# Kernel tuning notes

Measured on AMD Instinct MI355X. Metric: run time of the kernel, lower is better.

Reference implementation:

```python
import jax, jax.numpy as jnp
import numpy as np

B_, T_, IN_, H_, N_ = 16, 4096, 2, 256, 256
TWO_PI = 6.283185307179586


def setup_inputs() -> dict:
    key = jax.random.key(0)
    ks = jax.random.split(key, 12)
    x = jax.random.normal(ks[0], (B_, T_, IN_), dtype=jnp.float32)
    lengths = jax.random.randint(ks[1], (B_,), 1, T_ + 1)  # in [1, T]
    # canonical LRU param init (ring init for eigenvalues)
    u1 = jax.random.uniform(ks[2], (N_,))
    u2 = jax.random.uniform(ks[3], (N_,))
    nu_log = jnp.log(-0.5 * jnp.log(u1 * 0.75 + 0.25))          # |lam| in [0.5, 1)
    theta_log = jnp.log(u2 * TWO_PI + 1e-4)
    B_re = jax.random.normal(ks[4], (N_, IN_)) / np.sqrt(2 * IN_)
    B_im = jax.random.normal(ks[5], (N_, IN_)) / np.sqrt(2 * IN_)
    C_re = jax.random.normal(ks[6], (H_, N_)) / np.sqrt(N_)
    C_im = jax.random.normal(ks[7], (H_, N_)) / np.sqrt(N_)
    D = jax.random.normal(ks[8], (H_, IN_))
    Wh = jax.random.normal(ks[9], (1, H_)) / np.sqrt(H_)
    bh = jnp.zeros((1,), dtype=jnp.float32)
    return {"x": x, "lengths": lengths, "nu_log": nu_log.astype(jnp.float32),
            "theta_log": theta_log.astype(jnp.float32), "B_re": B_re.astype(jnp.float32),
            "B_im": B_im.astype(jnp.float32), "C_re": C_re.astype(jnp.float32),
            "C_im": C_im.astype(jnp.float32), "D": D.astype(jnp.float32),
            "Wh": Wh.astype(jnp.float32), "bh": bh}


def _combine(e1, e2):
    a1, b1 = e1
    a2, b2 = e2
    return a1 * a2, a2 * b1 + b2


def reference(x, lengths, nu_log, theta_log, B_re, B_im, C_re, C_im, D, Wh, bh):
    B, T, _ = x.shape
    lam = jnp.exp(-jnp.exp(nu_log) + 1j * jnp.exp(theta_log))          # [N] complex
    gamma = jnp.sqrt(1.0 - jnp.abs(lam) ** 2)                           # [N] real
    Bmat = (B_re + 1j * B_im) * gamma[:, None]                          # [N, IN]
    Bu = jnp.einsum('bti,ni->btn', x.astype(jnp.complex64), Bmat)       # [B,T,N]
    a = jnp.broadcast_to(lam.astype(jnp.complex64), Bu.shape)
    # parallel associative scan of x_t = lam*x_{t-1} + Bu_t along time
    _, states = jax.lax.associative_scan(_combine, (a, Bu), axis=1)     # [B,T,N]
    C = C_re + 1j * C_im                                                # [H,N]
    y = jnp.einsum('btn,hn->bth', states, C).real + x @ D.T             # [B,T,H]
    mask = (jnp.arange(T) < lengths[:, None])[..., None]                # [B,T,1]
    y = y * mask
    last = jnp.take_along_axis(y, (lengths - 1)[:, None, None], axis=1)[:, 0, :]  # [B,H]
    return last @ Wh.T + bh                                             # [B,1]
```

## Files before the change

kernel.cpp:

```cpp
#include <hip/hip_runtime.h>
#include <hip/hip_bf16.h>

#define B_ 16
#define T_ 4096
#define IN_ 2
#define H_ 256
#define N_ 256

#define TWO_PI_F 6.28318530717958647692f
#define INV_TWO_PI_D 0.15915494309189533576888376337251

__global__ __launch_bounds__(256) void cw_kernel(const float* __restrict__ C_re,
                                                 const float* __restrict__ C_im,
                                                 const float* __restrict__ Wh,
                                                 float2* __restrict__ Cw) {
    int n = blockIdx.x;
    int h = threadIdx.x;
    float w = Wh[h];
    float vr = w * C_re[h * N_ + n];
    float vi = w * C_im[h * N_ + n];
    for (int off = 32; off > 0; off >>= 1) {
        vr += __shfl_down(vr, off);
        vi += __shfl_down(vi, off);
    }
    __shared__ float2 sred[4];
    int wid = threadIdx.x >> 6;
    int lane = threadIdx.x & 63;
    if (lane == 0) sred[wid] = make_float2(vr, vi);
    __syncthreads();
    if (threadIdx.x == 0) {
        float2 t = sred[0];
        t.x += sred[1].x + sred[2].x + sred[3].x;
        t.y += sred[1].y + sred[2].y + sred[3].y;
        Cw[n] = t;
    }
}

__global__ __launch_bounds__(256) void lru_kernel(
        const float* __restrict__ x, const int* __restrict__ lengths,
        const float* __restrict__ nu_log, const float* __restrict__ theta_log,
        const float* __restrict__ B_re, const float* __restrict__ B_im,
        const float2* __restrict__ Cw, float* __restrict__ g) {
    const int n = blockIdx.x;
    const int b = blockIdx.y;
    const int tid = threadIdx.x;
    const int tstar = lengths[b] - 1;

    const float nu = __expf(nu_log[n]);
    const float th = __expf(theta_log[n]);
    const double threv = (double)th * INV_TWO_PI_D;

    const float2* xb = ((const float2*)x) + (size_t)b * T_;

    const int k0 = (tstar - tid) & 255;
    const int s0 = tstar - k0;

    double f0 = (double)k0 * threv;
    float ang0 = (float)(f0 - rint(f0)) * TWO_PI_F;
    float sn, cs;
    __sincosf(ang0, &sn, &cs);
    float e0 = __expf(-(float)k0 * nu);
    float fr = e0 * cs, fi = e0 * sn;
    double f2 = 256.0 * threv;
    float ang2 = (float)(f2 - rint(f2)) * TWO_PI_F;
    __sincosf(ang2, &sn, &cs);
    float e2 = __expf(-256.f * nu);
    float rr = e2 * cs, ri = e2 * sn;

    float a0r = 0.f, a0i = 0.f, a1r = 0.f, a1i = 0.f;
#pragma unroll
    for (int j = 0; j < 16; ++j) {
        int s = s0 - 256 * j;
        int sc = s < 0 ? 0 : s;
        float2 xv = xb[sc];
        if (s < 0) { xv.x = 0.f; xv.y = 0.f; }
        a0r = fmaf(fr, xv.x, a0r);
        a0i = fmaf(fi, xv.x, a0i);
        a1r = fmaf(fr, xv.y, a1r);
        a1i = fmaf(fi, xv.y, a1i);
        float nfr = fr * rr - fi * ri;
        float nfi = fmaf(fr, ri, fi * rr);
        fr = nfr;
        fi = nfi;
    }

    for (int off = 32; off > 0; off >>= 1) {
        a0r += __shfl_down(a0r, off);
        a0i += __shfl_down(a0i, off);
        a1r += __shfl_down(a1r, off);
        a1i += __shfl_down(a1i, off);
    }
    __shared__ float4 sred[4];
    int wid = threadIdx.x >> 6;
    int lane = threadIdx.x & 63;
    if (lane == 0) sred[wid] = make_float4(a0r, a0i, a1r, a1i);
    __syncthreads();
    if (threadIdx.x == 0) {
        float4 t = sred[0];
        t.x += sred[1].x + sred[2].x + sred[3].x;
        t.y += sred[1].y + sred[2].y + sred[3].y;
        t.z += sred[1].z + sred[2].z + sred[3].z;
        t.w += sred[1].w + sred[2].w + sred[3].w;
        float gamma = sqrtf(1.f - __expf(-2.f * nu));
        float br0 = B_re[2 * n] * gamma, bi0 = B_im[2 * n] * gamma;
        float br1 = B_re[2 * n + 1] * gamma, bi1 = B_im[2 * n + 1] * gamma;
        float str = t.x * br0 - t.y * bi0 + t.z * br1 - t.w * bi1;
        float sti = t.x * bi0 + t.y * br0 + t.z * bi1 + t.w * br1;
        float2 cw = Cw[n];
        g[b * N_ + n] = str * cw.x - sti * cw.y;
    }
}

__global__ __launch_bounds__(256) void out_kernel(
        const float* __restrict__ g, const float* __restrict__ x,
        const int* __restrict__ lengths, const float* __restrict__ D,
        const float* __restrict__ Wh, const float* __restrict__ bh,
        float* __restrict__ out) {
    int b = blockIdx.x;
    int tstar = lengths[b] - 1;
    int h = threadIdx.x;
    float2 xv = ((const float2*)x)[(size_t)b * T_ + tstar];
    float v = g[b * N_ + h] + Wh[h] * (D[2 * h] * xv.x + D[2 * h + 1] * xv.y);
    for (int off = 32; off > 0; off >>= 1) v += __shfl_down(v, off);
    __shared__ float sred[4];
    int wid = threadIdx.x >> 6;
    int lane = threadIdx.x & 63;
    if (lane == 0) sred[wid] = v;
    __syncthreads();
    if (threadIdx.x == 0) {
        out[b] = sred[0] + sred[1] + sred[2] + sred[3] + bh[0];
    }
}

extern "C" void kernel_launch(void* const* d_in, const int* in_sizes, int n_in,
                              void* d_out, int out_size, void* d_ws, size_t ws_size,
                              hipStream_t stream) {
    const float* x         = (const float*)d_in[0];
    const int*   lengths   = (const int*)d_in[1];
    const float* nu_log    = (const float*)d_in[2];
    const float* theta_log = (const float*)d_in[3];
    const float* B_re      = (const float*)d_in[4];
    const float* B_im      = (const float*)d_in[5];
    const float* C_re      = (const float*)d_in[6];
    const float* C_im      = (const float*)d_in[7];
    const float* D         = (const float*)d_in[8];
    const float* Wh        = (const float*)d_in[9];
    const float* bh        = (const float*)d_in[10];
    float* out = (float*)d_out;

    float2* Cw = (float2*)d_ws;
    float*  g  = (float*)d_ws + 2 * N_;

    cw_kernel<<<N_, 256, 0, stream>>>(C_re, C_im, Wh, Cw);
    lru_kernel<<<dim3(N_, B_), 256, 0, stream>>>(x, lengths, nu_log, theta_log,
                                                 B_re, B_im, Cw, g);
    out_kernel<<<B_, 256, 0, stream>>>(g, x, lengths, D, Wh, bh, out);
}
```

Baseline: 87.50 us.

## Fuse Cw reduction into LRU kernel and process two states per block

```diff
diff --git a/kernel.cpp b/kernel.cpp
--- a/kernel.cpp
+++ b/kernel.cpp
@@ -10,104 +10,117 @@
 #define TWO_PI_F 6.28318530717958647692f
 #define INV_TWO_PI_D 0.15915494309189533576888376337251
 
-__global__ __launch_bounds__(256) void cw_kernel(const float* __restrict__ C_re,
-                                                 const float* __restrict__ C_im,
-                                                 const float* __restrict__ Wh,
-                                                 float2* __restrict__ Cw) {
-    int n = blockIdx.x;
-    int h = threadIdx.x;
-    float w = Wh[h];
-    float vr = w * C_re[h * N_ + n];
-    float vi = w * C_im[h * N_ + n];
-    for (int off = 32; off > 0; off >>= 1) {
-        vr += __shfl_down(vr, off);
-        vi += __shfl_down(vi, off);
-    }
-    __shared__ float2 sred[4];
-    int wid = threadIdx.x >> 6;
-    int lane = threadIdx.x & 63;
-    if (lane == 0) sred[wid] = make_float2(vr, vi);
-    __syncthreads();
-    if (threadIdx.x == 0) {
-        float2 t = sred[0];
-        t.x += sred[1].x + sred[2].x + sred[3].x;
-        t.y += sred[1].y + sred[2].y + sred[3].y;
-        Cw[n] = t;
-    }
-}
-
-__global__ __launch_bounds__(256) void lru_kernel(
+__global__ __launch_bounds__(256) void lru_fused_kernel(
         const float* __restrict__ x, const int* __restrict__ lengths,
         const float* __restrict__ nu_log, const float* __restrict__ theta_log,
         const float* __restrict__ B_re, const float* __restrict__ B_im,
-        const float2* __restrict__ Cw, float* __restrict__ g) {
-    const int n = blockIdx.x;
+        const float* __restrict__ C_re, const float* __restrict__ C_im,
+        const float* __restrict__ Wh, float* __restrict__ g) {
+    const int n0 = blockIdx.x * 2;
+    const int n1 = n0 + 1;
     const int b = blockIdx.y;
     const int tid = threadIdx.x;
     const int tstar = lengths[b] - 1;
 
-    const float nu = __expf(nu_log[n]);
-    const float th = __expf(theta_log[n]);
-    const double threv = (double)th * INV_TWO_PI_D;
-
-    const float2* xb = ((const float2*)x) + (size_t)b * T_;
+    float w = Wh[tid];
+    float2 cre = *(const float2*)(C_re + tid * N_ + n0);
+    float2 cim = *(const float2*)(C_im + tid * N_ + n0);
+    float cw0r = w * cre.x, cw0i = w * cim.x;
+    float cw1r = w * cre.y, cw1i = w * cim.y;
 
     const int k0 = (tstar - tid) & 255;
     const int s0 = tstar - k0;
+    float sn, cs;
 
-    double f0 = (double)k0 * threv;
-    float ang0 = (float)(f0 - rint(f0)) * TWO_PI_F;
-    float sn, cs;
-    __sincosf(ang0, &sn, &cs);
-    float e0 = __expf(-(float)k0 * nu);
-    float fr = e0 * cs, fi = e0 * sn;
-    double f2 = 256.0 * threv;
-    float ang2 = (float)(f2 - rint(f2)) * TWO_PI_F;
-    __sincosf(ang2, &sn, &cs);
-    float e2 = __expf(-256.f * nu);
-    float rr = e2 * cs, ri = e2 * sn;
+    const float nu0 = __expf(nu_log[n0]);
+    const double thr0 = (double)__expf(theta_log[n0]) * INV_TWO_PI_D;
+    double f0 = (double)k0 * thr0;
+    __sincosf((float)(f0 - rint(f0)) * TWO_PI_F, &sn, &cs);
+    float e = __expf(-(float)k0 * nu0);
+    float fa_r = e * cs, fa_i = e * sn;
+    double q0 = 256.0 * thr0;
+    __sincosf((float)(q0 - rint(q0)) * TWO_PI_F, &sn, &cs);
+    e = __expf(-256.f * nu0);
+    const float ra_r = e * cs, ra_i = e * sn;
 
-    float a0r = 0.f, a0i = 0.f, a1r = 0.f, a1i = 0.f;
+    const float nu1 = __expf(nu_log[n1]);
+    const double thr1 = (double)__expf(theta_log[n1]) * INV_TWO_PI_D;
+    double f1 = (double)k0 * thr1;
+    __sincosf((float)(f1 - rint(f1)) * TWO_PI_F, &sn, &cs);
+    e = __expf(-(float)k0 * nu1);
+    float fb_r = e * cs, fb_i = e * sn;
+    double q1 = 256.0 * thr1;
+    __sincosf((float)(q1 - rint(q1)) * TWO_PI_F, &sn, &cs);
+    e = __expf(-256.f * nu1);
+    const float rb_r = e * cs, rb_i = e * sn;
+
+    const float2* xb = ((const float2*)x) + (size_t)b * T_;
+    float A0r = 0.f, A0i = 0.f, A1r = 0.f, A1i = 0.f;
+    float B0r = 0.f, B0i = 0.f, B1r = 0.f, B1i = 0.f;
 #pragma unroll
     for (int j = 0; j < 16; ++j) {
         int s = s0 - 256 * j;
         int sc = s < 0 ? 0 : s;
         float2 xv = xb[sc];
         if (s < 0) { xv.x = 0.f; xv.y = 0.f; }
-        a0r = fmaf(fr, xv.x, a0r);
-        a0i = fmaf(fi, xv.x, a0i);
-        a1r = fmaf(fr, xv.y, a1r);
-        a1i = fmaf(fi, xv.y, a1i);
-        float nfr = fr * rr - fi * ri;
-        float nfi = fmaf(fr, ri, fi * rr);
-        fr = nfr;
-        fi = nfi;
+        A0r = fmaf(fa_r, xv.x, A0r);
+        A0i = fmaf(fa_i, xv.x, A0i);
+        A1r = fmaf(fa_r, xv.y, A1r);
+        A1i = fmaf(fa_i, xv.y, A1i);
+        B0r = fmaf(fb_r, xv.x, B0r);
+        B0i = fmaf(fb_i, xv.x, B0i);
+        B1r = fmaf(fb_r, xv.y, B1r);
+        B1i = fmaf(fb_i, xv.y, B1i);
+        float t;
+        t = fa_r * ra_r - fa_i * ra_i;
+        fa_i = fmaf(fa_r, ra_i, fa_i * ra_r);
+        fa_r = t;
+        t = fb_r * rb_r - fb_i * rb_i;
+        fb_i = fmaf(fb_r, rb_i, fb_i * rb_r);
+        fb_r = t;
     }
 
     for (int off = 32; off > 0; off >>= 1) {
-        a0r += __shfl_down(a0r, off);
-        a0i += __shfl_down(a0i, off);
-        a1r += __shfl_down(a1r, off);
-        a1i += __shfl_down(a1i, off);
+        A0r += __shfl_down(A0r, off);
+        A0i += __shfl_down(A0i, off);
+        A1r += __shfl_down(A1r, off);
+        A1i += __shfl_down(A1i, off);
+        B0r += __shfl_down(B0r, off);
+        B0i += __shfl_down(B0i, off);
+        B1r += __shfl_down(B1r, off);
+        B1i += __shfl_down(B1i, off);
+        cw0r += __shfl_down(cw0r, off);
+        cw0i += __shfl_down(cw0i, off);
+        cw1r += __shfl_down(cw1r, off);
+        cw1i += __shfl_down(cw1i, off);
     }
-    __shared__ float4 sred[4];
-    int wid = threadIdx.x >> 6;
-    int lane = threadIdx.x & 63;
-    if (lane == 0) sred[wid] = make_float4(a0r, a0i, a1r, a1i);
+    __shared__ float sred[4][12];
+    int wid = tid >> 6;
+    int lane = tid & 63;
+    if (lane == 0) {
+        float* p = sred[wid];
+        p[0] = A0r;  p[1] = A0i;  p[2] = A1r;  p[3] = A1i;
+        p[4] = B0r;  p[5] = B0i;  p[6] = B1r;  p[7] = B1i;
+        p[8] = cw0r; p[9] = cw0i; p[10] = cw1r; p[11] = cw1i;
+    }
     __syncthreads();
-    if (threadIdx.x == 0) {
-        float4 t = sred[0];
-        t.x += sred[1].x + sred[2].x + sred[3].x;
-        t.y += sred[1].y + sred[2].y + sred[3].y;
-        t.z += sred[1].z + sred[2].z + sred[3].z;
-        t.w += sred[1].w + sred[2].w + sred[3].w;
+    if (tid < 2) {
+        int base = tid * 4;
+        float t0 = sred[0][base]     + sred[1][base]     + sred[2][base]     + sred[3][base];
+        float t1 = sred[0][base + 1] + sred[1][base + 1] + sred[2][base + 1] + sred[3][base + 1];
+        float t2 = sred[0][base + 2] + sred[1][base + 2] + sred[2][base + 2] + sred[3][base + 2];
+        float t3 = sred[0][base + 3] + sred[1][base + 3] + sred[2][base + 3] + sred[3][base + 3];
+        int cb = 8 + tid * 2;
+        float cwr = sred[0][cb]     + sred[1][cb]     + sred[2][cb]     + sred[3][cb];
+        float cwi = sred[0][cb + 1] + sred[1][cb + 1] + sred[2][cb + 1] + sred[3][cb + 1];
+        int n = n0 + tid;
+        float nu = __expf(nu_log[n]);
         float gamma = sqrtf(1.f - __expf(-2.f * nu));
         float br0 = B_re[2 * n] * gamma, bi0 = B_im[2 * n] * gamma;
         float br1 = B_re[2 * n + 1] * gamma, bi1 = B_im[2 * n + 1] * gamma;
-        float str = t.x * br0 - t.y * bi0 + t.z * br1 - t.w * bi1;
-        float sti = t.x * bi0 + t.y * br0 + t.z * bi1 + t.w * br1;
-        float2 cw = Cw[n];
-        g[b * N_ + n] = str * cw.x - sti * cw.y;
+        float str = t0 * br0 - t1 * bi0 + t2 * br1 - t3 * bi1;
+        float sti = t0 * bi0 + t1 * br0 + t2 * bi1 + t3 * br1;
+        g[b * N_ + n] = str * cwr - sti * cwi;
     }
 }
 
@@ -148,11 +161,9 @@
     const float* bh        = (const float*)d_in[10];
     float* out = (float*)d_out;
 
-    float2* Cw = (float2*)d_ws;
-    float*  g  = (float*)d_ws + 2 * N_;
+    float* g = (float*)d_ws;
 
-    cw_kernel<<<N_, 256, 0, stream>>>(C_re, C_im, Wh, Cw);
-    lru_kernel<<<dim3(N_, B_), 256, 0, stream>>>(x, lengths, nu_log, theta_log,
-                                                 B_re, B_im, Cw, g);
+    lru_fused_kernel<<<dim3(N_ / 2, B_), 256, 0, stream>>>(
+        x, lengths, nu_log, theta_log, B_re, B_im, C_re, C_im, Wh, g);
     out_kernel<<<B_, 256, 0, stream>>>(g, x, lengths, D, Wh, bh, out);
 }
```

New measurement: 86.17 us. No clear change (-1.5%).
